# Kernel optimization log

Measured on AMD Instinct MI355X. Metric: run time of the kernel, lower is better.

## Reference

```python
import jax, jax.numpy as jnp
import numpy as np

N_HEADS = 8
NEG = -1e9  # additive mask value standing in for -inf (bf16-safe)


def _mha(q_in, kv_in, w_in, b_in, w_out, b_out, mask):
    """torch nn.MultiheadAttention (batch_first, eval/no-dropout) equivalent.
    w_in: [3D, D] packed q/k/v in_proj weight, b_in: [3D]; w_out: [D, D], b_out: [D].
    mask: optional [L, L] additive mask.
    """
    B, Lq, D = q_in.shape
    H = N_HEADS
    dh = D // H
    Lk = kv_in.shape[1]
    q = q_in @ w_in[:D].T + b_in[:D]
    k = kv_in @ w_in[D:2 * D].T + b_in[D:2 * D]
    v = kv_in @ w_in[2 * D:].T + b_in[2 * D:]
    q = q.reshape(B, Lq, H, dh)
    k = k.reshape(B, Lk, H, dh)
    v = v.reshape(B, Lk, H, dh)
    scores = jnp.einsum('bqhd,bkhd->bhqk', q, k) / jnp.sqrt(jnp.asarray(dh, q.dtype))
    if mask is not None:
        scores = scores + mask  # broadcast [L,L] over [B,H,L,L]
    attn = jax.nn.softmax(scores, axis=-1)
    out = jnp.einsum('bhqk,bkhd->bqhd', attn, v).reshape(B, Lq, D)
    return out @ w_out.T + b_out


def _causal_mask(L):
    i = jnp.arange(L)
    return jnp.where(i[None, :] <= i[:, None], 0.0, NEG).astype(jnp.float32)


def _band_mask(L, window):
    # causal AND |i-j| <= window//2 (Eq. 13 band mask + causal mask)
    i = jnp.arange(L)
    diff = i[None, :] - i[:, None]  # key - query
    ok = (diff <= 0) & (jnp.abs(diff) <= window // 2)
    return jnp.where(ok, 0.0, NEG).astype(jnp.float32)


def setup_inputs() -> dict:
    key = jax.random.key(0)
    ks = jax.random.split(key, 10)
    B, L, D = 8, 1024, 512

    def rn(k, shape, scale=0.02):
        return jax.random.normal(k, shape, jnp.float32) * scale

    return {
        'user_emb': jax.random.normal(ks[0], (B, L, D), jnp.float32),
        'item_emb': jax.random.normal(ks[1], (B, L, D), jnp.float32),
        'attn_w_in': rn(ks[2], (6, 3 * D, D)),
        'attn_b_in': jnp.zeros((6, 3 * D), jnp.float32),
        'attn_w_out': rn(ks[3], (6, D, D)),
        'attn_b_out': jnp.zeros((6, D), jnp.float32),
        'cross_user_w': rn(ks[4], (D, D)),
        'cross_user_b': jnp.zeros((D,), jnp.float32),
        'cross_item_w': rn(ks[5], (D, D)),
        'cross_item_b': jnp.zeros((D,), jnp.float32),
        'gate_w': rn(ks[6], (2, D, 6)),
        'gate_b': jnp.zeros((2, 6), jnp.float32),
        'head_w1': rn(ks[7], (3, D, D // 2)),
        'head_b1': jnp.zeros((3, D // 2), jnp.float32),
        'head_w2': rn(ks[8], (3, D // 2)),
        'head_b2': jnp.zeros((3,), jnp.float32),
    }


def reference(user_emb, item_emb, attn_w_in, attn_b_in, attn_w_out, attn_b_out,
              cross_user_w, cross_user_b, cross_item_w, cross_item_b,
              gate_w, gate_b, head_w1, head_b1, head_w2, head_b2):
    B, L, D = item_emb.shape
    causal = _causal_mask(L)

    # 1) shared global causal SA (residual added by caller per docstring)
    shared = item_emb + _mha(item_emb, item_emb, attn_w_in[0], attn_b_in[0], attn_w_out[0], attn_b_out[0], causal)
    # 2) EXP-specific causal SA on shared output
    e_exp = shared + _mha(shared, shared, attn_w_in[1], attn_b_in[1], attn_w_out[1], attn_b_out[1], causal)
    # 3) CLK-specific causal SA on shared output
    e_clk = shared + _mha(shared, shared, attn_w_in[2], attn_b_in[2], attn_w_out[2], attn_b_out[2], causal)
    # 4) cross-attention: user queries into item keys/values (Eq. 12)
    u = user_emb @ cross_user_w.T + cross_user_b
    pv = item_emb @ cross_item_w.T + cross_item_b
    e_cross = _mha(u, pv, attn_w_in[3], attn_b_in[3], attn_w_out[3], attn_b_out[3], None)
    # 5/6) local (banded causal) self-attention, windows 4 and 6 (Eq. 13)
    e_lsa4 = item_emb + _mha(item_emb, item_emb, attn_w_in[4], attn_b_in[4], attn_w_out[4], attn_b_out[4], _band_mask(L, 4))
    e_lsa6 = item_emb + _mha(item_emb, item_emb, attn_w_in[5], attn_b_in[5], attn_w_out[5], attn_b_out[5], _band_mask(L, 6))

    experts = jnp.stack([shared, e_exp, e_clk, e_cross, e_lsa4, e_lsa6], axis=2)  # [B,L,6,D]
    # PLE gates: per-task softmax gate over the 6 experts conditioned on item_emb
    gate_logits = jnp.einsum('bld,tde->tble', item_emb, gate_w) + gate_b[:, None, None, :]
    gates = jax.nn.softmax(gate_logits, axis=-1)  # [2,B,L,6]
    h_exp = jnp.einsum('ble,bled->bld', gates[0], experts)
    h_clk = jnp.einsum('ble,bled->bld', gates[1], experts)

    def head(h, i):
        hid = jax.nn.relu(h @ head_w1[i] + head_b1[i])  # [B,L,D//2]
        return hid @ head_w2[i] + head_b2[i]  # [B,L]

    p_exp = jax.nn.sigmoid(head(h_exp, 0))
    p_clk = jax.nn.sigmoid(head(h_clk, 1))
    p_cvr = jax.nn.sigmoid(head(h_clk, 2))
    return (p_exp, p_clk, p_cvr)
```

## Files before the change

### kernel.cpp

```cpp
#include <hip/hip_runtime.h>
#include <hip/hip_bf16.h>
#include <stdint.h>


using bf16 = __hip_bfloat16;
typedef __attribute__((ext_vector_type(8))) short short8v;
typedef __attribute__((ext_vector_type(4))) short short4v;
typedef __attribute__((ext_vector_type(4))) float float4v;

#define LDK 40
#define LDKB 72
#define LQA 76
#define EXPC 0.18033688011112042f

__device__ __forceinline__ float wred_sum(float v) {
    #pragma unroll
    for (int off = 32; off; off >>= 1) v += __shfl_xor(v, off);
    return v;
}
__device__ __forceinline__ short f2bs(float x) {
    bf16 b = __float2bfloat16(x);
    return *reinterpret_cast<short*>(&b);
}
__device__ __forceinline__ float b2f(bf16 v) { return __bfloat162float(v); }

__global__ __launch_bounds__(256) void fillf_kernel(float* __restrict__ p, float v, int n) {
    const int i = blockIdx.x * 256 + threadIdx.x;
    if (i < n) p[i] = v;
}

__global__ __launch_bounds__(256) void cvt_all_kernel(
    const float* s0, bf16* d0, const float* s1, bf16* d1, const float* s2, bf16* d2,
    const float* s3, bf16* d3, const float* s4, bf16* d4, const float* s5, bf16* d5,
    const float* s6, bf16* d6)
{
    const int i = blockIdx.x * 256 + threadIdx.x;
    const float* src; bf16* dst; int off;
    if      (i < 1048576) { src = s0; dst = d0; off = i; }
    else if (i < 2097152) { src = s1; dst = d1; off = i - 1048576; }
    else if (i < 3276800) { src = s2; dst = d2; off = i - 2097152; }
    else if (i < 3670016) { src = s3; dst = d3; off = i - 3276800; }
    else if (i < 3735552) { src = s4; dst = d4; off = i - 3670016; }
    else if (i < 3801088) { src = s5; dst = d5; off = i - 3735552; }
    else if (i < 3899392) { src = s6; dst = d6; off = i - 3801088; }
    else return;
    const float4 v = *(const float4*)&src[(size_t)off << 2];
    short4v o;
    o[0] = f2bs(v.x); o[1] = f2bs(v.y); o[2] = f2bs(v.z); o[3] = f2bs(v.w);
    *(short4v*)&dst[(size_t)off << 2] = o;
}

__global__ __launch_bounds__(256) void gemm_bb_nt128(
    const bf16* __restrict__ X, const bf16* __restrict__ W,
    const float* __restrict__ bias, bf16* __restrict__ Yb, int ldY, int K)
{
    __shared__ short As[128 * LDKB];
    __shared__ short Bs[128 * LDKB];
    const int tid = threadIdx.x;
    const int lane = tid & 63, w = tid >> 6;
    const int wr = (w >> 1) << 6, wc = (w & 1) << 6;
    const int bm = blockIdx.y * 128, bn = blockIdx.x * 128;
    const int srow = tid >> 1, scol = (tid & 1) << 5;
    const int c16 = lane & 15, g16 = lane >> 4;

    float4v acc[4][4] = {};
    for (int k0 = 0; k0 < K; k0 += 64) {
        const bf16* xs = &X[(size_t)(bm + srow) * K + k0 + scol];
        const bf16* wsrc = &W[(size_t)(bn + srow) * K + k0 + scol];
        const short8v x0 = *(const short8v*)xs;
        const short8v x1 = *(const short8v*)(xs + 8);
        const short8v x2 = *(const short8v*)(xs + 16);
        const short8v x3 = *(const short8v*)(xs + 24);
        const short8v w0 = *(const short8v*)wsrc;
        const short8v w1 = *(const short8v*)(wsrc + 8);
        const short8v w2 = *(const short8v*)(wsrc + 16);
        const short8v w3 = *(const short8v*)(wsrc + 24);
        __syncthreads();
        *(short8v*)&As[srow * LDKB + scol]      = x0;
        *(short8v*)&As[srow * LDKB + scol + 8]  = x1;
        *(short8v*)&As[srow * LDKB + scol + 16] = x2;
        *(short8v*)&As[srow * LDKB + scol + 24] = x3;
        *(short8v*)&Bs[srow * LDKB + scol]      = w0;
        *(short8v*)&Bs[srow * LDKB + scol + 8]  = w1;
        *(short8v*)&Bs[srow * LDKB + scol + 16] = w2;
        *(short8v*)&Bs[srow * LDKB + scol + 24] = w3;
        __syncthreads();
        #pragma unroll
        for (int ks = 0; ks < 2; ++ks) {
            short8v af[4], bf4[4];
            #pragma unroll
            for (int i = 0; i < 4; ++i) {
                af[i]  = *(const short8v*)&As[(wr + (i << 4) + c16) * LDKB + (ks << 5) + (g16 << 3)];
                bf4[i] = *(const short8v*)&Bs[(wc + (i << 4) + c16) * LDKB + (ks << 5) + (g16 << 3)];
            }
            #pragma unroll
            for (int i = 0; i < 4; ++i)
                #pragma unroll
                for (int j = 0; j < 4; ++j)
                    acc[i][j] = __builtin_amdgcn_mfma_f32_16x16x32_bf16(af[i], bf4[j], acc[i][j], 0, 0, 0);
        }
    }
    #pragma unroll
    for (int i = 0; i < 4; ++i)
        #pragma unroll
        for (int rg = 0; rg < 4; ++rg) {
            const int m = bm + wr + (i << 4) + (g16 << 2) + rg;
            #pragma unroll
            for (int j = 0; j < 4; ++j) {
                const int n = bn + wc + (j << 4) + c16;
                Yb[(size_t)m * ldY + n] = __float2bfloat16(acc[i][j][rg] + bias[n]);
            }
        }
}

__global__ __launch_bounds__(256) void gemm_bb_nt(
    const bf16* __restrict__ X, const bf16* __restrict__ W,
    const float* __restrict__ bias, bf16* __restrict__ Yb, int ldY, int K)
{
    __shared__ short As[64 * LDK];
    __shared__ short Bs[64 * LDK];
    const int tid = threadIdx.x;
    const int lane = tid & 63, w = tid >> 6;
    const int bm = blockIdx.y * 64, bn = blockIdx.x * 64;
    const int r = tid >> 2, c8 = (tid & 3) << 3;
    const int arow = ((w << 4) + (lane & 15)) * LDK + ((lane >> 4) << 3);
    const int bbase = (lane & 15) * LDK + ((lane >> 4) << 3);

    float4v acc[4] = {};
    for (int k0 = 0; k0 < K; k0 += 32) {
        const short8v av = *(const short8v*)&X[(size_t)(bm + r) * K + k0 + c8];
        const short8v bv = *(const short8v*)&W[(size_t)(bn + r) * K + k0 + c8];
        __syncthreads();
        *(short8v*)&As[r * LDK + c8] = av;
        *(short8v*)&Bs[r * LDK + c8] = bv;
        __syncthreads();
        const short8v a = *(const short8v*)&As[arow];
        #pragma unroll
        for (int c = 0; c < 4; ++c) {
            const short8v b = *(const short8v*)&Bs[(c << 4) * LDK + bbase];
            acc[c] = __builtin_amdgcn_mfma_f32_16x16x32_bf16(a, b, acc[c], 0, 0, 0);
        }
    }
    #pragma unroll
    for (int rg = 0; rg < 4; ++rg) {
        const int m = bm + (w << 4) + ((lane >> 4) << 2) + rg;
        #pragma unroll
        for (int c = 0; c < 4; ++c) {
            const int n = bn + (c << 4) + (lane & 15);
            Yb[(size_t)m * ldY + n] = __float2bfloat16(acc[c][rg] + bias[n]);
        }
    }
}

__global__ __launch_bounds__(256) void gemm_bb_nt_dual(
    const bf16* __restrict__ XA, const bf16* __restrict__ WA, const float* __restrict__ biasA,
    const bf16* __restrict__ XB, const bf16* __restrict__ WB, const float* __restrict__ biasB,
    const bf16* __restrict__ resA, const bf16* __restrict__ resB,
    bf16* __restrict__ Yb, int ldY,
    bf16* __restrict__ h0, bf16* __restrict__ h1,
    const float* __restrict__ g, int eA, int eB, int hinit, int K)
{
    __shared__ short As[64 * LDK];
    __shared__ short Bs[64 * LDK];
    const int tid = threadIdx.x;
    const int lane = tid & 63, w = tid >> 6;
    const int bm = blockIdx.y * 64, bn = blockIdx.x * 64;
    const int r = tid >> 2, c8 = (tid & 3) << 3;
    const int arow = ((w << 4) + (lane & 15)) * LDK + ((lane >> 4) << 3);
    const int bbase = (lane & 15) * LDK + ((lane >> 4) << 3);

    float4v accA[4] = {};
    for (int k0 = 0; k0 < K; k0 += 32) {
        const short8v av = *(const short8v*)&XA[(size_t)(bm + r) * K + k0 + c8];
        const short8v bv = *(const short8v*)&WA[(size_t)(bn + r) * K + k0 + c8];
        __syncthreads();
        *(short8v*)&As[r * LDK + c8] = av;
        *(short8v*)&Bs[r * LDK + c8] = bv;
        __syncthreads();
        const short8v a = *(const short8v*)&As[arow];
        #pragma unroll
        for (int c = 0; c < 4; ++c) {
            const short8v b = *(const short8v*)&Bs[(c << 4) * LDK + bbase];
            accA[c] = __builtin_amdgcn_mfma_f32_16x16x32_bf16(a, b, accA[c], 0, 0, 0);
        }
    }
    float4v accB[4] = {};
    for (int k0 = 0; k0 < K; k0 += 32) {
        const short8v av = *(const short8v*)&XB[(size_t)(bm + r) * K + k0 + c8];
        const short8v bv = *(const short8v*)&WB[(size_t)(bn + r) * K + k0 + c8];
        __syncthreads();
        *(short8v*)&As[r * LDK + c8] = av;
        *(short8v*)&Bs[r * LDK + c8] = bv;
        __syncthreads();
        const short8v a = *(const short8v*)&As[arow];
        #pragma unroll
        for (int c = 0; c < 4; ++c) {
            const short8v b = *(const short8v*)&Bs[(c << 4) * LDK + bbase];
            accB[c] = __builtin_amdgcn_mfma_f32_16x16x32_bf16(a, b, accB[c], 0, 0, 0);
        }
    }
    #pragma unroll
    for (int rg = 0; rg < 4; ++rg) {
        const int m = bm + (w << 4) + ((lane >> 4) << 2) + rg;
        const float gA0 = g[(size_t)m * 6 + eA];
        const float gA1 = g[(size_t)(8192 + m) * 6 + eA];
        const float gB0 = g[(size_t)m * 6 + eB];
        const float gB1 = g[(size_t)(8192 + m) * 6 + eB];
        #pragma unroll
        for (int c = 0; c < 4; ++c) {
            const int n = bn + (c << 4) + (lane & 15);
            float vA = accA[c][rg] + biasA[n];
            if (resA) vA += b2f(resA[(size_t)m * 512 + n]);
            float vB = accB[c][rg] + biasB[n];
            if (resB) vB += b2f(resB[(size_t)m * 512 + n]);
            if (Yb) Yb[(size_t)m * ldY + n] = __float2bfloat16(vA);
            const size_t hi = (size_t)m * 512 + n;
            const float t0 = gA0 * vA + gB0 * vB;
            const float t1 = gA1 * vA + gB1 * vB;
            if (hinit) {
                h0[hi] = __float2bfloat16(t0);
                h1[hi] = __float2bfloat16(t1);
            } else {
                h0[hi] = __float2bfloat16(b2f(h0[hi]) + t0);
                h1[hi] = __float2bfloat16(b2f(h1[hi]) + t1);
            }
        }
    }
}

__global__ __launch_bounds__(256) void gemm_mfma_nn_relu(
    const bf16* __restrict__ X, const bf16* __restrict__ W,
    const float* __restrict__ bias, float* __restrict__ Y, int N, int K)
{
    __shared__ short As[64 * LDK];
    __shared__ short Bs[64 * LDK + 64];
    const int tid = threadIdx.x;
    const int lane = tid & 63, w = tid >> 6;
    const int bm = blockIdx.y * 64, bn = blockIdx.x * 64;
    const int r = tid >> 2, c8 = (tid & 3) << 3;
    const int kk = tid >> 3, nn0 = (tid & 7) << 3;
    const int arow = ((w << 4) + (lane & 15)) * LDK + ((lane >> 4) << 3);

    float4v acc[4] = {};
    for (int k0 = 0; k0 < K; k0 += 32) {
        const short8v av = *(const short8v*)&X[(size_t)(bm + r) * K + k0 + c8];
        const short8v bw = *(const short8v*)&W[(size_t)(k0 + kk) * N + bn + nn0];
        __syncthreads();
        *(short8v*)&As[r * LDK + c8] = av;
        #pragma unroll
        for (int i = 0; i < 8; ++i) {
            const int nn = nn0 + i;
            Bs[nn * LDK + ((nn >> 3) << 3) + kk] = bw[i];
        }
        __syncthreads();
        const short8v a = *(const short8v*)&As[arow];
        #pragma unroll
        for (int c = 0; c < 4; ++c) {
            const int n = (c << 4) + (lane & 15);
            const short8v b = *(const short8v*)&Bs[n * LDK + ((n >> 3) << 3) + ((lane >> 4) << 3)];
            acc[c] = __builtin_amdgcn_mfma_f32_16x16x32_bf16(a, b, acc[c], 0, 0, 0);
        }
    }
    #pragma unroll
    for (int rg = 0; rg < 4; ++rg) {
        const int m = bm + (w << 4) + ((lane >> 4) << 2) + rg;
        #pragma unroll
        for (int c = 0; c < 4; ++c) {
            const int n = bn + (c << 4) + (lane & 15);
            Y[(size_t)m * N + n] = fmaxf(acc[c][rg] + bias[n], 0.f);
        }
    }
}

__global__ __launch_bounds__(512) void attn_flash2(
    const bf16* __restrict__ q0, const bf16* __restrict__ k0, const bf16* __restrict__ v0,
    bf16* __restrict__ o0, int ld0, int c0,
    const bf16* __restrict__ q1, const bf16* __restrict__ k1, const bf16* __restrict__ v1,
    bf16* __restrict__ o1, int ld1, int c1, int L)
{
    const int half = blockIdx.y >> 3;
    int bq = blockIdx.y & 7;
    const bf16 *qb, *kb, *vb; bf16* out; int ld, causal;
    if (half == 0) { qb = q0; kb = k0; vb = v0; out = o0; ld = ld0; causal = c0; }
    else           { qb = q1; kb = k1; vb = v1; out = o1; ld = ld1; causal = c1; }
    if (causal) bq = (bq < 4) ? bq : (11 - bq);
    const int b = blockIdx.x >> 3, h = blockIdx.x & 7;
    const int tid = threadIdx.x;
    const int lane = tid & 63, w = tid >> 6;
    const int g16 = lane >> 4, c16 = lane & 15;
    __shared__ short Ks[64 * LQA];
    __shared__ short Ps[128 * LQA];
    __shared__ short Vt[64 * LQA + 64];
    const size_t base = (size_t)b * L * ld + (size_t)h * 64;
    const int qlo = bq << 7;

    short8v qa0, qa1;
    {
        const bf16* qsrc = qb + base + (size_t)(qlo + (w << 4) + c16) * ld + (g16 << 3);
        qa0 = *(const short8v*)qsrc;
        qa1 = *(const short8v*)(qsrc + 32);
    }

    const int sr2 = (tid & 255) >> 2, sc2 = (tid & 3) << 4;
    const bool isK = tid < 256;

    float4v oacc[4] = {};
    float lrow[4] = {0.f, 0.f, 0.f, 0.f};

    const int nkt = causal ? ((bq + 1) << 1) : (L >> 6);

    short8v pf0, pf1;
    {
        const bf16* src = (isK ? kb : vb) + base + (size_t)sr2 * ld + sc2;
        pf0 = *(const short8v*)src;
        pf1 = *(const short8v*)(src + 8);
    }

    for (int kt = 0; kt < nkt; ++kt) {
        const int klo = kt << 6;
        __syncthreads();
        if (isK) {
            *(short8v*)&Ks[sr2 * LQA + sc2]     = pf0;
            *(short8v*)&Ks[sr2 * LQA + sc2 + 8] = pf1;
        } else {
            #pragma unroll
            for (int i = 0; i < 8; ++i) Vt[(sc2 + i) * LQA + sc2 + sr2] = pf0[i];
            #pragma unroll
            for (int i = 0; i < 8; ++i) Vt[(sc2 + 8 + i) * LQA + sc2 + sr2] = pf1[i];
        }
        __syncthreads();
        if (kt + 1 < nkt) {
            const bf16* src = (isK ? kb : vb) + base + (size_t)(((kt + 1) << 6) + sr2) * ld + sc2;
            pf0 = *(const short8v*)src;
            pf1 = *(const short8v*)(src + 8);
        }
        float4v sacc[4] = {};
        #pragma unroll
        for (int ct = 0; ct < 4; ++ct) {
            const short8v b0 = *(const short8v*)&Ks[((ct << 4) + c16) * LQA + (g16 << 3)];
            sacc[ct] = __builtin_amdgcn_mfma_f32_16x16x32_bf16(qa0, b0, sacc[ct], 0, 0, 0);
            const short8v b1 = *(const short8v*)&Ks[((ct << 4) + c16) * LQA + 32 + (g16 << 3)];
            sacc[ct] = __builtin_amdgcn_mfma_f32_16x16x32_bf16(qa1, b1, sacc[ct], 0, 0, 0);
        }
        const bool diag = causal && (klo + 63 > qlo + (w << 4));
        #pragma unroll
        for (int ct = 0; ct < 4; ++ct)
            #pragma unroll
            for (int rg = 0; rg < 4; ++rg) {
                float p = exp2f(sacc[ct][rg] * EXPC);
                if (diag && (klo + (ct << 4) + c16) > (qlo + (w << 4) + (g16 << 2) + rg))
                    p = 0.f;
                lrow[rg] += p;
                Ps[((w << 4) + (g16 << 2) + rg) * LQA + (ct << 4) + c16] = f2bs(p);
            }
        #pragma unroll
        for (int ks = 0; ks < 2; ++ks) {
            const short8v a = *(const short8v*)&Ps[((w << 4) + c16) * LQA + (ks << 5) + (g16 << 3)];
            #pragma unroll
            for (int dt = 0; dt < 4; ++dt) {
                const short8v bf = *(const short8v*)&Vt[((dt << 4) + c16) * LQA + (dt << 4) + (ks << 5) + (g16 << 3)];
                oacc[dt] = __builtin_amdgcn_mfma_f32_16x16x32_bf16(a, bf, oacc[dt], 0, 0, 0);
            }
        }
    }
    #pragma unroll
    for (int rg = 0; rg < 4; ++rg) {
        float v = lrow[rg];
        #pragma unroll
        for (int off = 8; off; off >>= 1) v += __shfl_xor(v, off);
        lrow[rg] = v;
    }
    #pragma unroll
    for (int rg = 0; rg < 4; ++rg) {
        const int row = qlo + (w << 4) + (g16 << 2) + rg;
        const float inv = 1.f / lrow[rg];
        #pragma unroll
        for (int dt = 0; dt < 4; ++dt)
            out[((size_t)b * L + row) * 512 + h * 64 + (dt << 4) + c16] =
                __float2bfloat16(oacc[dt][rg] * inv);
    }
}

__global__ __launch_bounds__(256) void attn_band2(
    const bf16* __restrict__ qkv, bf16* __restrict__ oA, bf16* __restrict__ oB,
    int L, int ld, int wA, int wB)
{
    const int half = blockIdx.y >> 6;
    const int yy = blockIdx.y & 63;
    const int u = threadIdx.x >> 6, t = threadIdx.x & 63;
    const int i = blockIdx.x * 4 + u;
    const int b = yy >> 3, h = yy & 7;
    const bf16* qb = qkv + half * 1536;
    const bf16* kb = qb + 512;
    const bf16* vb = qb + 1024;
    bf16* out = half ? oB : oA;
    const int w = half ? wB : wA;
    const size_t base = (size_t)b * L * ld + (size_t)h * 64;
    const float qv = b2f(qb[base + (size_t)i * ld + t]);
    const int jmin = (i - w) > 0 ? (i - w) : 0;
    const int n = i - jmin;
    float sv[4];
    float mx = -1e30f;
    #pragma unroll
    for (int q = 0; q < 4; ++q) {
        float d = -1e30f;
        if (q <= n) {
            float dd = qv * b2f(kb[base + (size_t)(jmin + q) * ld + t]);
            d = wred_sum(dd) * 0.125f;
        }
        sv[q] = d;
        mx = fmaxf(mx, d);
    }
    float lsum = 0.f, acc = 0.f;
    #pragma unroll
    for (int q = 0; q < 4; ++q) {
        if (q <= n) {
            const float p = __expf(sv[q] - mx);
            lsum += p;
            acc += p * b2f(vb[base + (size_t)(jmin + q) * ld + t]);
        }
    }
    out[((size_t)b * L + i) * 512 + h * 64 + t] = __float2bfloat16(acc / lsum);
}

__global__ __launch_bounds__(64) void gates_v2(
    const float* __restrict__ item, const float* __restrict__ gw,
    const float* __restrict__ gb, float* __restrict__ g, int rows)
{
    const int r = blockIdx.x;
    const int t = threadIdx.x;
    __shared__ float xr[512];
    __shared__ float lg[12];
    for (int ii = t; ii < 512; ii += 64) xr[ii] = item[(size_t)r * 512 + ii];
    __syncthreads();
    #pragma unroll
    for (int p = 0; p < 12; ++p) {
        const int tk = p / 6, e = p % 6;
        float s = 0.f;
        #pragma unroll
        for (int dd = t; dd < 512; dd += 64) s += xr[dd] * gw[(size_t)(tk * 512 + dd) * 6 + e];
        s = wred_sum(s);
        if (t == 0) lg[p] = s + gb[p];
    }
    __syncthreads();
    if (t < 2) {
        float mx = -1e30f;
        #pragma unroll
        for (int e = 0; e < 6; ++e) mx = fmaxf(mx, lg[t * 6 + e]);
        float sum = 0.f, p6[6];
        #pragma unroll
        for (int e = 0; e < 6; ++e) { p6[e] = __expf(lg[t * 6 + e] - mx); sum += p6[e]; }
        #pragma unroll
        for (int e = 0; e < 6; ++e) g[(size_t)(t * rows + r) * 6 + e] = p6[e] / sum;
    }
}

__global__ __launch_bounds__(256) void head2_v2(
    const float* __restrict__ hid0, const float* __restrict__ hid1, const float* __restrict__ hid2,
    const float* __restrict__ w2, const float* __restrict__ b2, float* __restrict__ out)
{
    const int w = threadIdx.x >> 6, lane = threadIdx.x & 63;
    const int r = blockIdx.x * 4 + w;
    float s0 = 0.f, s1 = 0.f, s2 = 0.f;
    #pragma unroll
    for (int d = lane; d < 256; d += 64) {
        s0 += hid0[(size_t)r * 256 + d] * w2[d];
        s1 += hid1[(size_t)r * 256 + d] * w2[256 + d];
        s2 += hid2[(size_t)r * 256 + d] * w2[512 + d];
    }
    s0 = wred_sum(s0); s1 = wred_sum(s1); s2 = wred_sum(s2);
    if (lane == 0) {
        out[r]         = 1.f / (1.f + __expf(-(s0 + b2[0])));
        out[8192 + r]  = 1.f / (1.f + __expf(-(s1 + b2[1])));
        out[16384 + r] = 1.f / (1.f + __expf(-(s2 + b2[2])));
    }
}

extern "C" void kernel_launch(void* const* d_in, const int* in_sizes, int n_in,
                              void* d_out, int out_size, void* d_ws, size_t ws_size,
                              hipStream_t stream)
{
    float* out = (float*)d_out;
    const int* s = in_sizes;
    const bool dicto = n_in == 16 &&
        s[0] == 4194304 && s[1] == 4194304 && s[2] == 4718592 && s[3] == 9216 &&
        s[4] == 1572864 && s[5] == 3072 && s[6] == 262144 && s[7] == 512 &&
        s[8] == 262144 && s[9] == 512 && s[10] == 6144 && s[11] == 12 &&
        s[12] == 393216 && s[13] == 768 && s[14] == 768 && s[15] == 3;
    if (!dicto) {
        fillf_kernel<<<dim3(96), dim3(256), 0, stream>>>(out, 16384.0f, out_size);
        return;
    }

    const float* user  = (const float*)d_in[0];
    const float* item  = (const float*)d_in[1];
    const float* w_in  = (const float*)d_in[2];
    const float* b_in  = (const float*)d_in[3];
    const float* w_out = (const float*)d_in[4];
    const float* b_out = (const float*)d_in[5];
    const float* cuw   = (const float*)d_in[6];
    const float* cub   = (const float*)d_in[7];
    const float* ciw   = (const float*)d_in[8];
    const float* cib   = (const float*)d_in[9];
    const float* gw    = (const float*)d_in[10];
    const float* gb    = (const float*)d_in[11];
    const float* hw1   = (const float*)d_in[12];
    const float* hb1   = (const float*)d_in[13];
    const float* hw2   = (const float*)d_in[14];
    const float* hb2   = (const float*)d_in[15];

    const int L = 1024, M = 8192;
    float* ws = (float*)d_ws;
    bf16* qkvb     = (bf16*)ws;
    bf16* qkvc     = qkvb + (size_t)12582912;
    bf16* attnoutb = (bf16*)(ws + 12582912);
    bf16* attnout2 = (bf16*)(ws + 16777216);
    bf16* h0b      = (bf16*)(ws + 20971520);
    bf16* h1b      = (bf16*)(ws + 25165824);
    bf16* uBb      = (bf16*)(ws + 29360128);
    bf16* sharedb  = (bf16*)(ws + 31457280);
    bf16* pvBb     = (bf16*)(ws + 33554432);
    float* g       = ws + 41943040;
    bf16* itemb    = (bf16*)(ws + 42041344);
    bf16* userb    = (bf16*)(ws + 44138496);
    bf16* w_inb    = (bf16*)(ws + 46235648);
    bf16* w_outb   = (bf16*)(ws + 48594944);
    bf16* cuwb     = (bf16*)(ws + 49381376);
    bf16* ciwb     = (bf16*)(ws + 49512448);
    bf16* hw1b     = (bf16*)(ws + 49643520);
    float* hid0 = ws;
    float* hid1 = ws + (size_t)M * 256;
    float* hid2 = ws + (size_t)M * 512;
    bf16* BN = nullptr;

    const dim3 blk512(512), blk256(256), blk64(64);
    const dim3 gP1536(12, 64), gP3072(24, 64), gP1024(8, 64);
    const dim3 g512(8, 128), g256(4, 128);
    const dim3 gFA2(64, 16), gBA2(256, 128);

    cvt_all_kernel<<<dim3(15232), blk256, 0, stream>>>(
        item, itemb, user, userb, w_in, w_inb, w_out, w_outb,
        cuw, cuwb, ciw, ciwb, hw1, hw1b);

    gates_v2<<<dim3(M), blk64, 0, stream>>>(item, gw, gb, g, M);

    gemm_bb_nt128<<<gP1536, blk256, 0, stream>>>(itemb, w_inb, b_in, qkvb, 1536, 512);
    gemm_bb_nt<<<g512, blk256, 0, stream>>>(userb, cuwb, cub, uBb, 512, 512);
    gemm_bb_nt<<<g512, blk256, 0, stream>>>(itemb, ciwb, cib, pvBb, 512, 512);
    gemm_bb_nt<<<g512, blk256, 0, stream>>>(uBb, w_inb + (size_t)3 * 786432,
        b_in + 3 * 1536, qkvc, 1536, 512);
    gemm_bb_nt128<<<gP1024, blk256, 0, stream>>>(pvBb, w_inb + (size_t)3 * 786432 + 262144,
        b_in + 3 * 1536 + 512, qkvc + 512, 1536, 512);

    attn_flash2<<<gFA2, blk512, 0, stream>>>(
        qkvb, qkvb + 512, qkvb + 1024, attnoutb, 1536, 1,
        qkvc, qkvc + 512, qkvc + 1024, attnout2, 1536, 0, L);

    gemm_bb_nt_dual<<<g512, blk256, 0, stream>>>(
        attnoutb, w_outb, b_out,
        attnout2, w_outb + (size_t)3 * 262144, b_out + 3 * 512,
        itemb, BN, sharedb, 512, h0b, h1b, g, 0, 3, 1, 512);

    gemm_bb_nt128<<<gP3072, blk256, 0, stream>>>(sharedb, w_inb + (size_t)786432,
        b_in + 1536, qkvb, 3072, 512);
    attn_flash2<<<gFA2, blk512, 0, stream>>>(
        qkvb, qkvb + 512, qkvb + 1024, attnoutb, 3072, 1,
        qkvb + 1536, qkvb + 2048, qkvb + 2560, attnout2, 3072, 1, L);
    gemm_bb_nt_dual<<<g512, blk256, 0, stream>>>(
        attnoutb, w_outb + 262144, b_out + 512,
        attnout2, w_outb + 524288, b_out + 1024,
        sharedb, sharedb, BN, 0, h0b, h1b, g, 1, 2, 0, 512);

    gemm_bb_nt128<<<gP3072, blk256, 0, stream>>>(itemb, w_inb + (size_t)4 * 786432,
        b_in + 4 * 1536, qkvb, 3072, 512);
    attn_band2<<<gBA2, blk256, 0, stream>>>(qkvb, attnoutb, attnout2, L, 3072, 2, 3);
    gemm_bb_nt_dual<<<g512, blk256, 0, stream>>>(
        attnoutb, w_outb + (size_t)4 * 262144, b_out + 4 * 512,
        attnout2, w_outb + (size_t)5 * 262144, b_out + 5 * 512,
        itemb, itemb, BN, 0, h0b, h1b, g, 4, 5, 0, 512);

    gemm_mfma_nn_relu<<<g256, blk256, 0, stream>>>(h0b, hw1b, hb1, hid0, 256, 512);
    gemm_mfma_nn_relu<<<g256, blk256, 0, stream>>>(h1b, hw1b + 131072, hb1 + 256, hid1, 256, 512);
    gemm_mfma_nn_relu<<<g256, blk256, 0, stream>>>(h1b, hw1b + 262144, hb1 + 512, hid2, 256, 512);
    head2_v2<<<dim3(2048), blk256, 0, stream>>>(hid0, hid1, hid2, hw2, hb2, out);
}
```

Baseline: 561.1 us.

## Compose cross projection into attention in-proj weights and batch head GEMMs

```diff
diff --git a/kernel.cpp b/kernel.cpp
--- a/kernel.cpp
+++ b/kernel.cpp
@@ -50,6 +50,67 @@
     *(short4v*)&dst[(size_t)off << 2] = o;
 }
 
+__global__ __launch_bounds__(256) void gemm_nn_compose(
+    const bf16* __restrict__ A, const bf16* __restrict__ B0, const bf16* __restrict__ B1,
+    bf16* __restrict__ Y)
+{
+    const int K = 512, N = 512;
+    __shared__ short As[64 * LDK];
+    __shared__ short Bs[64 * LDK + 64];
+    const int tid = threadIdx.x;
+    const int lane = tid & 63, w = tid >> 6;
+    const int bm = blockIdx.y * 64, bn = blockIdx.x * 64;
+    const bf16* B = (bm < 512) ? B0 : B1;
+    const int r = tid >> 2, c8 = (tid & 3) << 3;
+    const int kk = tid >> 3, nn0 = (tid & 7) << 3;
+    const int arow = ((w << 4) + (lane & 15)) * LDK + ((lane >> 4) << 3);
+
+    float4v acc[4] = {};
+    for (int k0 = 0; k0 < K; k0 += 32) {
+        const short8v av = *(const short8v*)&A[(size_t)(bm + r) * K + k0 + c8];
+        const short8v bw = *(const short8v*)&B[(size_t)(k0 + kk) * N + bn + nn0];
+        __syncthreads();
+        *(short8v*)&As[r * LDK + c8] = av;
+        #pragma unroll
+        for (int i = 0; i < 8; ++i) {
+            const int nn = nn0 + i;
+            Bs[nn * LDK + ((nn >> 3) << 3) + kk] = bw[i];
+        }
+        __syncthreads();
+        const short8v a = *(const short8v*)&As[arow];
+        #pragma unroll
+        for (int c = 0; c < 4; ++c) {
+            const int n = (c << 4) + (lane & 15);
+            const short8v b = *(const short8v*)&Bs[n * LDK + ((n >> 3) << 3) + ((lane >> 4) << 3)];
+            acc[c] = __builtin_amdgcn_mfma_f32_16x16x32_bf16(a, b, acc[c], 0, 0, 0);
+        }
+    }
+    #pragma unroll
+    for (int rg = 0; rg < 4; ++rg) {
+        const int m = bm + (w << 4) + ((lane >> 4) << 2) + rg;
+        #pragma unroll
+        for (int c = 0; c < 4; ++c) {
+            const int n = bn + (c << 4) + (lane & 15);
+            Y[(size_t)m * N + n] = __float2bfloat16(acc[c][rg]);
+        }
+    }
+}
+
+__global__ __launch_bounds__(256) void compose_bias_kernel(
+    const float* __restrict__ w3f, const float* __restrict__ cub,
+    const float* __restrict__ cib, const float* __restrict__ b3f,
+    float* __restrict__ bo)
+{
+    const int wid = threadIdx.x >> 6, lane = threadIdx.x & 63;
+    const int n = blockIdx.x * 4 + wid;
+    const float* cv = (n < 512) ? cub : cib;
+    float s = 0.f;
+    #pragma unroll
+    for (int k = lane; k < 512; k += 64) s += w3f[(size_t)n * 512 + k] * cv[k];
+    s = wred_sum(s);
+    if (lane == 0) bo[n] = s + b3f[n];
+}
+
 __global__ __launch_bounds__(256) void gemm_bb_nt128(
     const bf16* __restrict__ X, const bf16* __restrict__ W,
     const float* __restrict__ bias, bf16* __restrict__ Yb, int ldY, int K)
@@ -113,9 +174,77 @@
         }
 }
 
-__global__ __launch_bounds__(256) void gemm_bb_nt(
-    const bf16* __restrict__ X, const bf16* __restrict__ W,
+__global__ __launch_bounds__(256) void gemm_bb_nt128_selX(
+    const bf16* __restrict__ X0, const bf16* __restrict__ X1, const bf16* __restrict__ W,
     const float* __restrict__ bias, bf16* __restrict__ Yb, int ldY, int K)
+{
+    __shared__ short As[128 * LDKB];
+    __shared__ short Bs[128 * LDKB];
+    const int tid = threadIdx.x;
+    const int lane = tid & 63, w = tid >> 6;
+    const int wr = (w >> 1) << 6, wc = (w & 1) << 6;
+    const int bm = blockIdx.y * 128, bn = blockIdx.x * 128;
+    const bf16* X = (bn < 512) ? X0 : X1;
+    const int srow = tid >> 1, scol = (tid & 1) << 5;
+    const int c16 = lane & 15, g16 = lane >> 4;
+
+    float4v acc[4][4] = {};
+    for (int k0 = 0; k0 < K; k0 += 64) {
+        const bf16* xs = &X[(size_t)(bm + srow) * K + k0 + scol];
+        const bf16* wsrc = &W[(size_t)(bn + srow) * K + k0 + scol];
+        const short8v x0 = *(const short8v*)xs;
+        const short8v x1 = *(const short8v*)(xs + 8);
+        const short8v x2 = *(const short8v*)(xs + 16);
+        const short8v x3 = *(const short8v*)(xs + 24);
+        const short8v w0 = *(const short8v*)wsrc;
+        const short8v w1 = *(const short8v*)(wsrc + 8);
+        const short8v w2 = *(const short8v*)(wsrc + 16);
+        const short8v w3 = *(const short8v*)(wsrc + 24);
+        __syncthreads();
+        *(short8v*)&As[srow * LDKB + scol]      = x0;
+        *(short8v*)&As[srow * LDKB + scol + 8]  = x1;
+        *(short8v*)&As[srow * LDKB + scol + 16] = x2;
+        *(short8v*)&As[srow * LDKB + scol + 24] = x3;
+        *(short8v*)&Bs[srow * LDKB + scol]      = w0;
+        *(short8v*)&Bs[srow * LDKB + scol + 8]  = w1;
+        *(short8v*)&Bs[srow * LDKB + scol + 16] = w2;
+        *(short8v*)&Bs[srow * LDKB + scol + 24] = w3;
+        __syncthreads();
+        #pragma unroll
+        for (int ks = 0; ks < 2; ++ks) {
+            short8v af[4], bf4[4];
+            #pragma unroll
+            for (int i = 0; i < 4; ++i) {
+                af[i]  = *(const short8v*)&As[(wr + (i << 4) + c16) * LDKB + (ks << 5) + (g16 << 3)];
+                bf4[i] = *(const short8v*)&Bs[(wc + (i << 4) + c16) * LDKB + (ks << 5) + (g16 << 3)];
+            }
+            #pragma unroll
+            for (int i = 0; i < 4; ++i)
+                #pragma unroll
+                for (int j = 0; j < 4; ++j)
+                    acc[i][j] = __builtin_amdgcn_mfma_f32_16x16x32_bf16(af[i], bf4[j], acc[i][j], 0, 0, 0);
+        }
+    }
+    #pragma unroll
+    for (int i = 0; i < 4; ++i)
+        #pragma unroll
+        for (int rg = 0; rg < 4; ++rg) {
+            const int m = bm + wr + (i << 4) + (g16 << 2) + rg;
+            #pragma unroll
+            for (int j = 0; j < 4; ++j) {
+                const int n = bn + wc + (j << 4) + c16;
+                Yb[(size_t)m * ldY + n] = __float2bfloat16(acc[i][j][rg] + bias[n]);
+            }
+        }
+}
+
+__global__ __launch_bounds__(256) void gemm_bb_nt_dual(
+    const bf16* __restrict__ XA, const bf16* __restrict__ WA, const float* __restrict__ biasA,
+    const bf16* __restrict__ XB, const bf16* __restrict__ WB, const float* __restrict__ biasB,
+    const bf16* __restrict__ resA, int resSame,
+    bf16* __restrict__ Yb, int ldY,
+    bf16* __restrict__ h0, bf16* __restrict__ h1,
+    const float* __restrict__ g, int eA, int eB, int hinit, int K)
 {
     __shared__ short As[64 * LDK];
     __shared__ short Bs[64 * LDK];
@@ -126,49 +255,6 @@
     const int arow = ((w << 4) + (lane & 15)) * LDK + ((lane >> 4) << 3);
     const int bbase = (lane & 15) * LDK + ((lane >> 4) << 3);
 
-    float4v acc[4] = {};
-    for (int k0 = 0; k0 < K; k0 += 32) {
-        const short8v av = *(const short8v*)&X[(size_t)(bm + r) * K + k0 + c8];
-        const short8v bv = *(const short8v*)&W[(size_t)(bn + r) * K + k0 + c8];
-        __syncthreads();
-        *(short8v*)&As[r * LDK + c8] = av;
-        *(short8v*)&Bs[r * LDK + c8] = bv;
-        __syncthreads();
-        const short8v a = *(const short8v*)&As[arow];
-        #pragma unroll
-        for (int c = 0; c < 4; ++c) {
-            const short8v b = *(const short8v*)&Bs[(c << 4) * LDK + bbase];
-            acc[c] = __builtin_amdgcn_mfma_f32_16x16x32_bf16(a, b, acc[c], 0, 0, 0);
-        }
-    }
-    #pragma unroll
-    for (int rg = 0; rg < 4; ++rg) {
-        const int m = bm + (w << 4) + ((lane >> 4) << 2) + rg;
-        #pragma unroll
-        for (int c = 0; c < 4; ++c) {
-            const int n = bn + (c << 4) + (lane & 15);
-            Yb[(size_t)m * ldY + n] = __float2bfloat16(acc[c][rg] + bias[n]);
-        }
-    }
-}
-
-__global__ __launch_bounds__(256) void gemm_bb_nt_dual(
-    const bf16* __restrict__ XA, const bf16* __restrict__ WA, const float* __restrict__ biasA,
-    const bf16* __restrict__ XB, const bf16* __restrict__ WB, const float* __restrict__ biasB,
-    const bf16* __restrict__ resA, const bf16* __restrict__ resB,
-    bf16* __restrict__ Yb, int ldY,
-    bf16* __restrict__ h0, bf16* __restrict__ h1,
-    const float* __restrict__ g, int eA, int eB, int hinit, int K)
-{
-    __shared__ short As[64 * LDK];
-    __shared__ short Bs[64 * LDK];
-    const int tid = threadIdx.x;
-    const int lane = tid & 63, w = tid >> 6;
-    const int bm = blockIdx.y * 64, bn = blockIdx.x * 64;
-    const int r = tid >> 2, c8 = (tid & 3) << 3;
-    const int arow = ((w << 4) + (lane & 15)) * LDK + ((lane >> 4) << 3);
-    const int bbase = (lane & 15) * LDK + ((lane >> 4) << 3);
-
     float4v accA[4] = {};
     for (int k0 = 0; k0 < K; k0 += 32) {
         const short8v av = *(const short8v*)&XA[(size_t)(bm + r) * K + k0 + c8];
@@ -209,10 +295,10 @@
         #pragma unroll
         for (int c = 0; c < 4; ++c) {
             const int n = bn + (c << 4) + (lane & 15);
-            float vA = accA[c][rg] + biasA[n];
-            if (resA) vA += b2f(resA[(size_t)m * 512 + n]);
-            float vB = accB[c][rg] + biasB[n];
-            if (resB) vB += b2f(resB[(size_t)m * 512 + n]);
+            float rv = 0.f;
+            if (resA) rv = b2f(resA[(size_t)m * 512 + n]);
+            float vA = accA[c][rg] + biasA[n] + rv;
+            float vB = accB[c][rg] + biasB[n] + (resSame ? rv : 0.f);
             if (Yb) Yb[(size_t)m * ldY + n] = __float2bfloat16(vA);
             const size_t hi = (size_t)m * 512 + n;
             const float t0 = gA0 * vA + gB0 * vB;
@@ -228,15 +314,23 @@
     }
 }
 
-__global__ __launch_bounds__(256) void gemm_mfma_nn_relu(
-    const bf16* __restrict__ X, const bf16* __restrict__ W,
-    const float* __restrict__ bias, float* __restrict__ Y, int N, int K)
-{
+__global__ __launch_bounds__(256) void gemm_mfma_nn_relu3(
+    const bf16* __restrict__ h0b, const bf16* __restrict__ h1b,
+    const bf16* __restrict__ hw1b, const float* __restrict__ hb1,
+    float* __restrict__ hid0, float* __restrict__ hid1, float* __restrict__ hid2)
+{
+    const int K = 512, N = 256;
+    const int seg = blockIdx.y >> 7;
+    const int by = blockIdx.y & 127;
+    const bf16* X = (seg == 0) ? h0b : h1b;
+    const bf16* W = hw1b + (size_t)seg * 131072;
+    const float* bias = hb1 + seg * 256;
+    float* Y = (seg == 0) ? hid0 : ((seg == 1) ? hid1 : hid2);
     __shared__ short As[64 * LDK];
     __shared__ short Bs[64 * LDK + 64];
     const int tid = threadIdx.x;
     const int lane = tid & 63, w = tid >> 6;
-    const int bm = blockIdx.y * 64, bn = blockIdx.x * 64;
+    const int bm = by * 64, bn = blockIdx.x * 64;
     const int r = tid >> 2, c8 = (tid & 3) << 3;
     const int kk = tid >> 3, nn0 = (tid & 7) << 3;
     const int arow = ((w << 4) + (lane & 15)) * LDK + ((lane >> 4) << 3);
@@ -517,9 +611,7 @@
     bf16* attnout2 = (bf16*)(ws + 16777216);
     bf16* h0b      = (bf16*)(ws + 20971520);
     bf16* h1b      = (bf16*)(ws + 25165824);
-    bf16* uBb      = (bf16*)(ws + 29360128);
     bf16* sharedb  = (bf16*)(ws + 31457280);
-    bf16* pvBb     = (bf16*)(ws + 33554432);
     float* g       = ws + 41943040;
     bf16* itemb    = (bf16*)(ws + 42041344);
     bf16* userb    = (bf16*)(ws + 44138496);
@@ -528,14 +620,16 @@
     bf16* cuwb     = (bf16*)(ws + 49381376);
     bf16* ciwb     = (bf16*)(ws + 49512448);
     bf16* hw1b     = (bf16*)(ws + 49643520);
+    bf16* Wcomp    = (bf16*)(ws + 49840128);
+    float* bcomp   = ws + 50233344;
     float* hid0 = ws;
     float* hid1 = ws + (size_t)M * 256;
     float* hid2 = ws + (size_t)M * 512;
     bf16* BN = nullptr;
 
     const dim3 blk512(512), blk256(256), blk64(64);
-    const dim3 gP1536(12, 64), gP3072(24, 64), gP1024(8, 64);
-    const dim3 g512(8, 128), g256(4, 128);
+    const dim3 gP1536(12, 64), gP3072(24, 64);
+    const dim3 g512(8, 128);
     const dim3 gFA2(64, 16), gBA2(256, 128);
 
     cvt_all_kernel<<<dim3(15232), blk256, 0, stream>>>(
@@ -544,13 +638,13 @@
 
     gates_v2<<<dim3(M), blk64, 0, stream>>>(item, gw, gb, g, M);
 
+    gemm_nn_compose<<<dim3(8, 24), blk256, 0, stream>>>(
+        w_inb + (size_t)3 * 786432, cuwb, ciwb, Wcomp);
+    compose_bias_kernel<<<dim3(384), blk256, 0, stream>>>(
+        w_in + (size_t)3 * 786432, cub, cib, b_in + 3 * 1536, bcomp);
+
     gemm_bb_nt128<<<gP1536, blk256, 0, stream>>>(itemb, w_inb, b_in, qkvb, 1536, 512);
-    gemm_bb_nt<<<g512, blk256, 0, stream>>>(userb, cuwb, cub, uBb, 512, 512);
-    gemm_bb_nt<<<g512, blk256, 0, stream>>>(itemb, ciwb, cib, pvBb, 512, 512);
-    gemm_bb_nt<<<g512, blk256, 0, stream>>>(uBb, w_inb + (size_t)3 * 786432,
-        b_in + 3 * 1536, qkvc, 1536, 512);
-    gemm_bb_nt128<<<gP1024, blk256, 0, stream>>>(pvBb, w_inb + (size_t)3 * 786432 + 262144,
-        b_in + 3 * 1536 + 512, qkvc + 512, 1536, 512);
+    gemm_bb_nt128_selX<<<gP1536, blk256, 0, stream>>>(userb, itemb, Wcomp, bcomp, qkvc, 1536, 512);
 
     attn_flash2<<<gFA2, blk512, 0, stream>>>(
         qkvb, qkvb + 512, qkvb + 1024, attnoutb, 1536, 1,
@@ -559,7 +653,7 @@
     gemm_bb_nt_dual<<<g512, blk256, 0, stream>>>(
         attnoutb, w_outb, b_out,
         attnout2, w_outb + (size_t)3 * 262144, b_out + 3 * 512,
-        itemb, BN, sharedb, 512, h0b, h1b, g, 0, 3, 1, 512);
+        itemb, 0, sharedb, 512, h0b, h1b, g, 0, 3, 1, 512);
 
     gemm_bb_nt128<<<gP3072, blk256, 0, stream>>>(sharedb, w_inb + (size_t)786432,
         b_in + 1536, qkvb, 3072, 512);
@@ -569,7 +663,7 @@
     gemm_bb_nt_dual<<<g512, blk256, 0, stream>>>(
         attnoutb, w_outb + 262144, b_out + 512,
         attnout2, w_outb + 524288, b_out + 1024,
-        sharedb, sharedb, BN, 0, h0b, h1b, g, 1, 2, 0, 512);
+        sharedb, 1, BN, 0, h0b, h1b, g, 1, 2, 0, 512);
 
     gemm_bb_nt128<<<gP3072, blk256, 0, stream>>>(itemb, w_inb + (size_t)4 * 786432,
         b_in + 4 * 1536, qkvb, 3072, 512);
@@ -577,10 +671,9 @@
     gemm_bb_nt_dual<<<g512, blk256, 0, stream>>>(
         attnoutb, w_outb + (size_t)4 * 262144, b_out + 4 * 512,
         attnout2, w_outb + (size_t)5 * 262144, b_out + 5 * 512,
-        itemb, itemb, BN, 0, h0b, h1b, g, 4, 5, 0, 512);
-
-    gemm_mfma_nn_relu<<<g256, blk256, 0, stream>>>(h0b, hw1b, hb1, hid0, 256, 512);
-    gemm_mfma_nn_relu<<<g256, blk256, 0, stream>>>(h1b, hw1b + 131072, hb1 + 256, hid1, 256, 512);
-    gemm_mfma_nn_relu<<<g256, blk256, 0, stream>>>(h1b, hw1b + 262144, hb1 + 512, hid2, 256, 512);
+        itemb, 1, BN, 0, h0b, h1b, g, 4, 5, 0, 512);
+
+    gemm_mfma_nn_relu3<<<dim3(4, 384), blk256, 0, stream>>>(
+        h0b, h1b, hw1b, hb1, hid0, hid1, hid2);
     head2_v2<<<dim3(2048), blk256, 0, stream>>>(hid0, hid1, hid2, hw2, hb2, out);
 }
```

New measurement: 520.0 us. -7.3%, faster.
